# Kernel tuning notes

Measured on AMD Instinct MI355X. Metric: run time of the kernel, lower is better.

The kernel has to match this reference:

```python
import jax, jax.numpy as jnp
import numpy as np

N_NODES = 256
IN_FEATURES = 4096
OUT_FEATURES = 7
LAYERS = 4
WIRES = 8                      # ceil(log2(n_nodes))
DIM = 2 ** WIRES               # state-vector length = 256
P2 = WIRES * (WIRES - 1) // 2  # 28 controlled gates per block
N_W = 6 * WIRES + 3 * P2       # 132 weights per layer (matches weight_shape)
CPLX = jnp.complex64
# op2_all_layers ordering: gaps 1..w-1, then j
PAIRS = [(j, j + gap) for gap in range(1, WIRES) for j in range(WIRES - gap)]


def _ry(t):
    c, s = jnp.cos(t / 2), jnp.sin(t / 2)
    return jnp.stack([jnp.stack([c, -s]), jnp.stack([s, c])]).astype(CPLX)


def _rx(t):
    c = jnp.cos(t / 2).astype(CPLX)
    s = (-1j * jnp.sin(t / 2)).astype(CPLX)
    return jnp.stack([jnp.stack([c, s]), jnp.stack([s, c])])


def _rz(t):
    z = jnp.zeros((), CPLX)
    return jnp.stack([jnp.stack([jnp.exp(-0.5j * t).astype(CPLX), z]),
                      jnp.stack([z, jnp.exp(0.5j * t).astype(CPLX)])])


# Constant-angle gates (the source passes the integer weight index as the
# controlled-rotation angle, so these are compile-time numpy constants).
def _ry_np(a):
    c, s = np.cos(a / 2), np.sin(a / 2)
    return np.array([[c, -s], [s, c]], np.complex64)


def _rx_np(a):
    c, s = np.cos(a / 2), np.sin(a / 2)
    return np.array([[c, -1j * s], [-1j * s, c]], np.complex64)


def _rz_np(a):
    return np.diag([np.exp(-0.5j * a), np.exp(0.5j * a)]).astype(np.complex64)


def apply_1q(state, M, q):
    # state: [B] + [2]*WIRES; wire q lives on axis q+1 (wire 0 = MSB, PennyLane order)
    s = jnp.moveaxis(state, q + 1, -1)
    s = jnp.einsum('...b,ab->...a', s, M)
    return jnp.moveaxis(s, -1, q + 1)


def apply_c1q(state, M, c, t):
    # controlled gate: apply M on target wire t in the control==1 subspace
    s = jnp.moveaxis(state, (c + 1, t + 1), (-2, -1))
    s1 = jnp.einsum('...b,ab->...a', s[..., 1, :], M)
    s = jnp.stack([s[..., 0, :], s1], axis=-2)
    return jnp.moveaxis(s, (-2, -1), (c + 1, t + 1))


def q_layer(state, wv):
    # Faithful port of the source q_layer, including the quirk that the
    # CRY/CRX/CRZ angles are the integer running weight index (constants).
    wi = 0
    for q in range(WIRES):
        state = apply_1q(state, _ry(wv[wi + q]), q)
    wi += WIRES
    for i, (c, t) in enumerate(PAIRS):
        state = apply_c1q(state, _ry_np(float(wi + i)), c, t)
    wi += P2
    for q in range(WIRES):
        state = apply_1q(state, _ry(wv[wi + q]), q)
    wi += WIRES
    for q in range(WIRES):
        state = apply_1q(state, _rx(wv[wi + q]), q)
    wi += WIRES
    for i, (c, t) in enumerate(PAIRS):
        state = apply_c1q(state, _rx_np(float(wi + i)), c, t)
    wi += P2
    for q in range(WIRES):
        state = apply_1q(state, _rx(wv[wi + q]), q)
    wi += WIRES
    for q in range(WIRES):
        state = apply_1q(state, _rz(wv[wi + q]), q)
    wi += WIRES
    for i, (c, t) in enumerate(PAIRS):
        state = apply_c1q(state, _rz_np(float(wi + i)), c, t)
    wi += P2
    for q in range(WIRES):
        state = apply_1q(state, _rz(wv[wi + q]), q)
    return state


def circuit(samples, qweights):
    # samples: [B, N_NODES] real -> AmplitudeEmbedding(pad_with=0, normalize=True)
    B = samples.shape[0]
    v = samples
    if DIM > N_NODES:
        v = jnp.pad(v, ((0, 0), (0, DIM - N_NODES)))
    v = v / jnp.linalg.norm(v, axis=1, keepdims=True)
    state = v.astype(CPLX).reshape((B,) + (2,) * WIRES)
    layer = jax.checkpoint(q_layer)  # bounds residual memory under AD
    for l in range(LAYERS):
        state = layer(state, qweights[l])
    p = state.real ** 2 + state.imag ** 2  # probabilities, [B] + [2]*WIRES
    zs = []
    for q in range(WIRES):
        axes = tuple(a for a in range(1, WIRES + 1) if a != q + 1)
        m = p.sum(axis=axes)            # [B, 2]
        zs.append(m[:, 0] - m[:, 1])    # <Z_q> = P(0) - P(1)
    return jnp.stack(zs, axis=1)        # [B, WIRES]


def setup_inputs() -> dict:
    key = jax.random.key(0)
    k1, k2, k3, k4 = jax.random.split(key, 4)
    x = jax.random.normal(k1, (N_NODES, IN_FEATURES), jnp.float32)
    qweights = jax.random.uniform(k2, (LAYERS, N_W), jnp.float32, 0.0, 2.0 * np.pi)
    fc_w = jax.random.normal(k3, (OUT_FEATURES, WIRES), jnp.float32) / np.sqrt(WIRES)
    fc_b = jax.random.normal(k4, (OUT_FEATURES,), jnp.float32) / np.sqrt(WIRES)
    return {"x": x, "qweights": qweights, "fc_w": fc_w, "fc_b": fc_b}


def reference(x, qweights, fc_w, fc_b):
    z = circuit(x.T, qweights)      # [IN_FEATURES, WIRES]
    return z @ fc_w.T + fc_b        # [IN_FEATURES, OUT_FEATURES]
```

## Files before the change

kernel.cpp:

```cpp
#include <hip/hip_runtime.h>
#include <math.h>


namespace {

constexpr int NSAMP = 4096;
constexpr int NW_L  = 132;

constexpr double PI_D   = 3.14159265358979323846264338327950288;
constexpr double TWO_PI = 6.28318530717958647692528676655900577;

constexpr double red_pm_pi(double x) {
  double k = x / TWO_PI;
  long long ki = (long long)k;
  double r = x - (double)ki * TWO_PI;
  if (r > PI_D)  r -= TWO_PI;
  if (r < -PI_D) r += TWO_PI;
  return r;
}
constexpr double csin(double x) {
  double r = red_pm_pi(x), r2 = r * r, term = r, sum = r;
  for (int n = 1; n <= 13; ++n) { term *= -r2 / (double)((2*n)*(2*n+1)); sum += term; }
  return sum;
}
constexpr double ccos(double x) {
  double r = red_pm_pi(x), r2 = r * r, term = 1.0, sum = 1.0;
  for (int n = 1; n <= 13; ++n) { term *= -r2 / (double)((2*n-1)*(2*n)); sum += term; }
  return sum;
}

constexpr int PC[28] = {0,1,2,3,4,5,6, 0,1,2,3,4,5, 0,1,2,3,4, 0,1,2,3, 0,1,2, 0,1, 0};
constexpr int PT[28] = {1,2,3,4,5,6,7, 2,3,4,5,6,7, 3,4,5,6,7, 4,5,6,7, 5,6,7, 6,7, 7};

struct Tbl28 { float c[28]; float s[28]; };
constexpr Tbl28 mk_tbl(int base) {
  Tbl28 t{};
  for (int i = 0; i < 28; ++i) {
    double a = 0.5 * (double)(base + i);
    t.c[i] = (float)ccos(a);
    t.s[i] = (float)csin(a);
  }
  return t;
}
constexpr Tbl28 T_CRY = mk_tbl(8);
constexpr Tbl28 T_CRX = mk_tbl(52);

struct DTbl { float v[512]; };
constexpr DTbl mk_dcrz() {
  DTbl t{};
  for (int s = 0; s < 256; ++s) {
    double psi = 0.0;
    for (int i = 0; i < 28; ++i) {
      const int pc = 7 - PC[i], pt = 7 - PT[i];
      if ((s >> pc) & 1) {
        const double half = 0.5 * (double)(96 + i);
        psi += ((s >> pt) & 1) ? half : -half;
      }
    }
    t.v[2*s]   = (float)ccos(psi);
    t.v[2*s+1] = (float)csin(psi);
  }
  return t;
}
__device__ constexpr DTbl D_CRZ = mk_dcrz();

__device__ __forceinline__ float shx(float v, int sh) {
  if (sh == 0) {
    int r = __builtin_amdgcn_update_dpp((int)__float_as_uint(v), (int)__float_as_uint(v),
                                        0xB1, 0xF, 0xF, true);
    return __uint_as_float((unsigned)r);
  }
  if (sh == 1) {
    int r = __builtin_amdgcn_update_dpp((int)__float_as_uint(v), (int)__float_as_uint(v),
                                        0x4E, 0xF, 0xF, true);
    return __uint_as_float((unsigned)r);
  }
  return __shfl_xor(v, 1 << sh, 64);
}

__device__ __forceinline__ void gen_cross(float* ar, float* ai, int lane, int sh,
                                          float m00r, float m00i, float m01r, float m01i) {
  const int bbit = (lane >> sh) & 1;
  const float dr = m00r;
  const float di = bbit ? -m00i : m00i;
  const float g  = bbit ? -m01r : m01r;
  const float h  = m01i;
#pragma unroll
  for (int r = 0; r < 4; ++r) {
    float pr = shx(ar[r], sh);
    float pi = shx(ai[r], sh);
    float mr = ar[r], mi = ai[r];
    ar[r] = dr*mr - di*mi + g*pr - h*pi;
    ai[r] = dr*mi + di*mr + g*pi + h*pr;
  }
}
__device__ __forceinline__ void gen_local(float* ar, float* ai, int p,
                                          float m00r, float m00i, float m01r, float m01i) {
  const int m = 1 << p;
#pragma unroll
  for (int r0 = 0; r0 < 4; ++r0) {
    if (!(r0 & m)) {
      const int r1 = r0 | m;
      float a0r=ar[r0], a0i=ai[r0], a1r=ar[r1], a1i=ai[r1];
      ar[r0] =  m00r*a0r - m00i*a0i + m01r*a1r - m01i*a1i;
      ai[r0] =  m00r*a0i + m00i*a0r + m01r*a1i + m01i*a1r;
      ar[r1] = -m01r*a0r - m01i*a0i + m00r*a1r + m00i*a1i;
      ai[r1] = -m01r*a0i + m01i*a0r + m00r*a1i - m00i*a1r;
    }
  }
}
__device__ __forceinline__ void cry_cross(float* ar, float* ai, int lane,
                                          int shc, int sht, float cc, float sc) {
  const int ctrl = (lane >> shc) & 1;
  const float ce = ctrl ? cc : 1.0f;
  float se = ((lane >> sht) & 1) ? sc : -sc;
  se = ctrl ? se : 0.0f;
#pragma unroll
  for (int r = 0; r < 4; ++r) {
    float pr = shx(ar[r], sht);
    float pi = shx(ai[r], sht);
    ar[r] = ce*ar[r] + se*pr;
    ai[r] = ce*ai[r] + se*pi;
  }
}
__device__ __forceinline__ void cry_local(float* ar, float* ai, int lane,
                                          int shc, int pt, float cc, float sc) {
  const int ctrl = (lane >> shc) & 1;
  const float ce = ctrl ? cc : 1.0f;
  const float se = ctrl ? sc : 0.0f;
  const int m = 1 << pt;
#pragma unroll
  for (int r0 = 0; r0 < 4; ++r0) {
    if (!(r0 & m)) {
      const int r1 = r0 | m;
      float a0r=ar[r0], a0i=ai[r0], a1r=ar[r1], a1i=ai[r1];
      ar[r0] = ce*a0r - se*a1r;  ai[r0] = ce*a0i - se*a1i;
      ar[r1] = ce*a1r + se*a0r;  ai[r1] = ce*a1i + se*a0i;
    }
  }
}
__device__ __forceinline__ void ry_pair23(float* ar, float* ai, float cc, float sc) {
  float a0r=ar[2], a0i=ai[2], a1r=ar[3], a1i=ai[3];
  ar[2] = cc*a0r - sc*a1r;  ai[2] = cc*a0i - sc*a1i;
  ar[3] = cc*a1r + sc*a0r;  ai[3] = cc*a1i + sc*a0i;
}
__device__ __forceinline__ void crx_cross(float* ar, float* ai, int lane,
                                          int shc, int sht, float cc, float sc) {
  const int ctrl = (lane >> shc) & 1;
  const float ce = ctrl ? cc : 1.0f;
  const float se = ctrl ? sc : 0.0f;
#pragma unroll
  for (int r = 0; r < 4; ++r) {
    float pr = shx(ar[r], sht);
    float pi = shx(ai[r], sht);
    ar[r] = ce*ar[r] + se*pi;
    ai[r] = ce*ai[r] - se*pr;
  }
}
__device__ __forceinline__ void crx_local(float* ar, float* ai, int lane,
                                          int shc, int pt, float cc, float sc) {
  const int ctrl = (lane >> shc) & 1;
  const float ce = ctrl ? cc : 1.0f;
  const float se = ctrl ? sc : 0.0f;
  const int m = 1 << pt;
#pragma unroll
  for (int r0 = 0; r0 < 4; ++r0) {
    if (!(r0 & m)) {
      const int r1 = r0 | m;
      float a0r=ar[r0], a0i=ai[r0], a1r=ar[r1], a1i=ai[r1];
      ar[r0] = ce*a0r + se*a1i;  ai[r0] = ce*a0i - se*a1r;
      ar[r1] = ce*a1r + se*a0i;  ai[r1] = ce*a1i - se*a0r;
    }
  }
}
__device__ __forceinline__ void rx_pair23(float* ar, float* ai, float cc, float sc) {
  float a0r=ar[2], a0i=ai[2], a1r=ar[3], a1i=ai[3];
  ar[2] = cc*a0r + sc*a1i;  ai[2] = cc*a0i - sc*a1r;
  ar[3] = cc*a1r + sc*a0i;  ai[3] = cc*a1i - sc*a0r;
}

__device__ __forceinline__ unsigned short f2bf(float f) {
  unsigned int u = __float_as_uint(f);
  u = (u + 0x7FFFu + ((u >> 16) & 1u)) >> 16;
  return (unsigned short)u;
}

typedef __attribute__((ext_vector_type(8))) short bf16x8;
typedef __attribute__((ext_vector_type(4))) float f32x4;

}

__global__ __launch_bounds__(64) void build_half(const float* __restrict__ qw,
                                                 float* __restrict__ U1c,
                                                 float* __restrict__ U2c) {
  __shared__ float4 sM[48];
  const int lane = threadIdx.x;
  const int h    = blockIdx.x >> 8;
  const int s0   = blockIdx.x & 255;

  if (lane < 48) {
    const int lp  = lane / 24;
    const int rem = lane - lp * 24;
    const int j   = rem >> 3;
    const int q   = rem & 7;
    const int l   = 2 * h + lp;
    float a, bb;
    if (j == 0) {
      a  = qw[l * NW_L + q];
      bb = (l > 0) ? qw[(l - 1) * NW_L + 124 + q] : 0.f;
    } else if (j == 1) {
      a  = qw[l * NW_L + 44 + q];
      bb = qw[l * NW_L + 36 + q];
    } else {
      a  = (l < 3) ? qw[l * NW_L + 88 + q] : 0.f;
      bb = qw[l * NW_L + 80 + q];
    }
    float sa, ca, sb, cb;
    __sincosf(0.5f * a,  &sa, &ca);
    __sincosf(0.5f * bb, &sb, &cb);
    float4 m;
    if (j == 0)      m = make_float4(ca*cb, -ca*sb, -sa*cb, -sa*sb);
    else if (j == 1) m = make_float4(ca*cb, -sa*sb, -ca*sb, -sa*cb);
    else             m = make_float4(ca*cb, -sa*cb, -sb*sa, -sb*ca);
    sM[lane] = m;
  }

  float ar[4], ai[4];
#pragma unroll
  for (int r = 0; r < 4; ++r) {
    ar[r] = (((lane << 2) | r) == s0) ? 1.f : 0.f;
    ai[r] = 0.f;
  }
  float dzr[4], dzi[4];
#pragma unroll
  for (int r = 0; r < 4; ++r) {
    const int s = (lane << 2) | r;
    dzr[r] = D_CRZ.v[2*s];
    dzi[r] = D_CRZ.v[2*s+1];
  }
  __syncthreads();

#pragma unroll 1
  for (int lp = 0; lp < 2; ++lp) {
    const int base = lp * 24;
#pragma unroll
    for (int q = 0; q < 8; ++q) {
      float4 m = sM[base + q];
      if (q <= 5) gen_cross(ar, ai, lane, 5 - q, m.x, m.y, m.z, m.w);
      else        gen_local(ar, ai, 7 - q, m.x, m.y, m.z, m.w);
    }
#pragma unroll
    for (int i = 0; i < 28; ++i) {
      const int c = PC[i], t = PT[i];
      const float cc = T_CRY.c[i], sc = T_CRY.s[i];
      if (t <= 5)      cry_cross(ar, ai, lane, 5 - c, 5 - t, cc, sc);
      else if (c <= 5) cry_local(ar, ai, lane, 5 - c, 7 - t, cc, sc);
      else             ry_pair23(ar, ai, cc, sc);
    }
#pragma unroll
    for (int q = 0; q < 8; ++q) {
      float4 m = sM[base + 8 + q];
      if (q <= 5) gen_cross(ar, ai, lane, 5 - q, m.x, m.y, m.z, m.w);
      else        gen_local(ar, ai, 7 - q, m.x, m.y, m.z, m.w);
    }
#pragma unroll
    for (int i = 0; i < 28; ++i) {
      const int c = PC[i], t = PT[i];
      const float cc = T_CRX.c[i], sc = T_CRX.s[i];
      if (t <= 5)      crx_cross(ar, ai, lane, 5 - c, 5 - t, cc, sc);
      else if (c <= 5) crx_local(ar, ai, lane, 5 - c, 7 - t, cc, sc);
      else             rx_pair23(ar, ai, cc, sc);
    }
#pragma unroll
    for (int q = 0; q < 8; ++q) {
      float4 m = sM[base + 16 + q];
      if (q <= 5) gen_cross(ar, ai, lane, 5 - q, m.x, m.y, m.z, m.w);
      else        gen_local(ar, ai, 7 - q, m.x, m.y, m.z, m.w);
    }
    if (2 * h + lp < 3) {
#pragma unroll
      for (int r = 0; r < 4; ++r) {
        float mr = ar[r], mi = ai[r];
        ar[r] = mr*dzr[r] - mi*dzi[r];
        ai[r] = mr*dzi[r] + mi*dzr[r];
      }
    }
  }

  float* Uc = h ? U2c : U1c;
  float4* dst = (float4*)(Uc + (size_t)s0 * 512);
  dst[2*lane]     = make_float4(ar[0], ai[0], ar[1], ai[1]);
  dst[2*lane + 1] = make_float4(ar[2], ai[2], ar[3], ai[3]);
}

__global__ __launch_bounds__(256) void combine_u(const float* __restrict__ U1c,
                                                 const float* __restrict__ U2c,
                                                 unsigned short* __restrict__ Ubf) {
  __shared__ float2 S2[32 * 16];
  __shared__ float2 S1[16 * 33];
  const int tid = threadIdx.x;
  const int ti  = tid & 15;
  const int tj  = tid >> 4;
  const int bi  = blockIdx.x & 15;
  const int bj  = blockIdx.x >> 4;

  float accr = 0.f, acci = 0.f;
#pragma unroll 1
  for (int kt = 0; kt < 8; ++kt) {
    __syncthreads();
#pragma unroll
    for (int v = 0; v < 2; ++v) {
      const int s = v * 256 + tid;
      const int k  = s >> 4, i = s & 15;
      S2[k * 16 + i] = *(const float2*)(U2c + (size_t)(kt*32 + k) * 512 + (bi*16 + i) * 2);
      const int j2 = s >> 5, k2 = s & 31;
      S1[j2 * 33 + k2] = *(const float2*)(U1c + (size_t)(bj*16 + j2) * 512 + (kt*32 + k2) * 2);
    }
    __syncthreads();
#pragma unroll
    for (int kk = 0; kk < 32; ++kk) {
      const float2 a = S2[kk * 16 + ti];
      const float2 b = S1[tj * 33 + kk];
      accr = fmaf(a.x, b.x, accr);  accr = fmaf(-a.y, b.y, accr);
      acci = fmaf(a.x, b.y, acci);  acci = fmaf(a.y, b.x, acci);
    }
  }
  const int i = bi * 16 + ti, j = bj * 16 + tj;
  Ubf[(size_t)i * 256 + j]         = f2bf(accr);
  Ubf[(size_t)(i + 256) * 256 + j] = f2bf(acci);
}

__global__ __launch_bounds__(1024) void eval3(const float* __restrict__ x,
                                              const unsigned short* __restrict__ Ubf,
                                              const float* __restrict__ fcw,
                                              const float* __restrict__ fcb,
                                              float* __restrict__ out) {
  __shared__ unsigned short Xs[16 * 264];
  __shared__ float Zp[16][16][9];
  __shared__ float Zf[16][9];
  const int tid  = threadIdx.x;
  const int lane = tid & 63;
  const int w    = tid >> 6;
  const int colbase = blockIdx.x * 16;

  {
    const int k  = tid >> 2;
    const int c4 = (tid & 3) * 4;
    const float4 v = *(const float4*)(x + (size_t)k * NSAMP + colbase + c4);
    Xs[(c4 + 0) * 264 + k] = f2bf(v.x);
    Xs[(c4 + 1) * 264 + k] = f2bf(v.y);
    Xs[(c4 + 2) * 264 + k] = f2bf(v.z);
    Xs[(c4 + 3) * 264 + k] = f2bf(v.w);
  }
  __syncthreads();

  const int quad = lane >> 4;
  const int n    = lane & 15;
  const int rowb = w * 32;

  f32x4 acc[2];
  acc[0] = (f32x4){0.f, 0.f, 0.f, 0.f};
  acc[1] = (f32x4){0.f, 0.f, 0.f, 0.f};

#pragma unroll
  for (int kt = 0; kt < 8; ++kt) {
    const bf16x8 bfrag = *(const bf16x8*)&Xs[n * 264 + kt * 32 + quad * 8];
#pragma unroll
    for (int rt = 0; rt < 2; ++rt) {
      const int row = rowb + rt * 16 + n;
      const bf16x8 afrag = *(const bf16x8*)(Ubf + (size_t)row * 256 + kt * 32 + quad * 8);
      acc[rt] = __builtin_amdgcn_mfma_f32_16x16x32_bf16(afrag, bfrag, acc[rt], 0, 0, 0);
    }
  }

  float za[9];
#pragma unroll
  for (int i = 0; i < 9; ++i) za[i] = 0.f;
  const float m4 = (lane & 32) ? -1.f : 1.f;
  const float m5 = (lane & 16) ? -1.f : 1.f;
#pragma unroll
  for (int rt = 0; rt < 2; ++rt) {
#pragma unroll
    for (int reg = 0; reg < 4; ++reg) {
      const float v = acc[rt][reg];
      const float p = v * v;
      za[0] += p;
      za[1] += (w & 4)   ? -p : p;
      za[2] += (w & 2)   ? -p : p;
      za[3] += (w & 1)   ? -p : p;
      za[4] += rt        ? -p : p;
      za[5] = fmaf(m4, p, za[5]);
      za[6] = fmaf(m5, p, za[6]);
      za[7] += (reg & 2) ? -p : p;
      za[8] += (reg & 1) ? -p : p;
    }
  }
#pragma unroll
  for (int off = 16; off <= 32; off <<= 1) {
#pragma unroll
    for (int i = 0; i < 9; ++i) za[i] += __shfl_xor(za[i], off, 64);
  }
  if (lane < 16) {
#pragma unroll
    for (int i = 0; i < 9; ++i) Zp[w][lane][i] = za[i];
  }
  __syncthreads();

  if (tid < 144) {
    const int col = tid / 9, q = tid - col * 9;
    float z = 0.f;
#pragma unroll
    for (int ww = 0; ww < 16; ++ww) z += Zp[ww][col][q];
    Zf[col][q] = z;
  }
  __syncthreads();

  if (tid < 112) {
    const int col = tid / 7, oo = tid - col * 7;
    const float inv = 1.f / Zf[col][0];
    float v = fcb[oo];
#pragma unroll
    for (int q = 0; q < 8; ++q)
      v = fmaf(fcw[oo * 8 + q], Zf[col][1 + q] * inv, v);
    out[(size_t)(colbase + col) * 7 + oo] = v;
  }
}

extern "C" void kernel_launch(void* const* d_in, const int* in_sizes, int n_in,
                              void* d_out, int out_size, void* d_ws, size_t ws_size,
                              hipStream_t stream) {
  const float* x   = (const float*)d_in[0];
  const float* qw  = (const float*)d_in[1];
  const float* fcw = (const float*)d_in[2];
  const float* fcb = (const float*)d_in[3];
  float* out = (float*)d_out;

  float* U1c = (float*)d_ws;
  float* U2c = U1c + 256 * 512;
  unsigned short* Ubf = (unsigned short*)(U2c + 256 * 512);

  hipLaunchKernelGGL(build_half, dim3(512), dim3(64),   0, stream, qw, U1c, U2c);
  hipLaunchKernelGGL(combine_u,  dim3(256), dim3(256),  0, stream, U1c, U2c, Ubf);
  hipLaunchKernelGGL(eval3,      dim3(256), dim3(1024), 0, stream, x, Ubf, fcw, fcb, out);
}
```

Before: 94.84 us.

## Drop combine kernel by chaining two half-unitary GEMMs inside eval

Instead of multiplying the two half-circuit unitaries into a full unitary in a separate fp32 kernel, the build kernel now writes U1 as bf16 and U2 as a real 512x512 block matrix that encodes the complex product. The eval kernel applies U1 to the input tile with MFMA, stores the bf16 intermediate in shared memory, then applies the 512-wide W2. This removes one launch and the scalar fp32 complex matmul. In exchange, eval does three times the MFMA work and reads a larger matrix, and the extra bf16 rounding of the intermediate state adds error. The build kernel's transposed scattered 2-byte stores may also be poorly coalesced.

```diff
diff --git a/kernel.cpp b/kernel.cpp
--- a/kernel.cpp
+++ b/kernel.cpp
@@ -190,9 +190,9 @@
 
 }
 
-__global__ __launch_bounds__(64) void build_half(const float* __restrict__ qw,
-                                                 float* __restrict__ U1c,
-                                                 float* __restrict__ U2c) {
+__global__ __launch_bounds__(64) void build_emit(const float* __restrict__ qw,
+                                                 unsigned short* __restrict__ U1bf,
+                                                 unsigned short* __restrict__ W2bf) {
   __shared__ float4 sM[48];
   const int lane = threadIdx.x;
   const int h    = blockIdx.x >> 8;
@@ -287,55 +287,33 @@
     }
   }
 
-  float* Uc = h ? U2c : U1c;
-  float4* dst = (float4*)(Uc + (size_t)s0 * 512);
-  dst[2*lane]     = make_float4(ar[0], ai[0], ar[1], ai[1]);
-  dst[2*lane + 1] = make_float4(ar[2], ai[2], ar[3], ai[3]);
-}
-
-__global__ __launch_bounds__(256) void combine_u(const float* __restrict__ U1c,
-                                                 const float* __restrict__ U2c,
-                                                 unsigned short* __restrict__ Ubf) {
-  __shared__ float2 S2[32 * 16];
-  __shared__ float2 S1[16 * 33];
-  const int tid = threadIdx.x;
-  const int ti  = tid & 15;
-  const int tj  = tid >> 4;
-  const int bi  = blockIdx.x & 15;
-  const int bj  = blockIdx.x >> 4;
-
-  float accr = 0.f, acci = 0.f;
-#pragma unroll 1
-  for (int kt = 0; kt < 8; ++kt) {
-    __syncthreads();
-#pragma unroll
-    for (int v = 0; v < 2; ++v) {
-      const int s = v * 256 + tid;
-      const int k  = s >> 4, i = s & 15;
-      S2[k * 16 + i] = *(const float2*)(U2c + (size_t)(kt*32 + k) * 512 + (bi*16 + i) * 2);
-      const int j2 = s >> 5, k2 = s & 31;
-      S1[j2 * 33 + k2] = *(const float2*)(U1c + (size_t)(bj*16 + j2) * 512 + (kt*32 + k2) * 2);
-    }
-    __syncthreads();
-#pragma unroll
-    for (int kk = 0; kk < 32; ++kk) {
-      const float2 a = S2[kk * 16 + ti];
-      const float2 b = S1[tj * 33 + kk];
-      accr = fmaf(a.x, b.x, accr);  accr = fmaf(-a.y, b.y, accr);
-      acci = fmaf(a.x, b.y, acci);  acci = fmaf(a.y, b.x, acci);
-    }
-  }
-  const int i = bi * 16 + ti, j = bj * 16 + tj;
-  Ubf[(size_t)i * 256 + j]         = f2bf(accr);
-  Ubf[(size_t)(i + 256) * 256 + j] = f2bf(acci);
-}
-
-__global__ __launch_bounds__(1024) void eval3(const float* __restrict__ x,
-                                              const unsigned short* __restrict__ Ubf,
-                                              const float* __restrict__ fcw,
-                                              const float* __restrict__ fcb,
-                                              float* __restrict__ out) {
+  if (h == 0) {
+#pragma unroll
+    for (int r = 0; r < 4; ++r) {
+      const int o = (lane << 2) | r;
+      U1bf[(size_t)o * 256 + s0]         = f2bf(ar[r]);
+      U1bf[(size_t)(o + 256) * 256 + s0] = f2bf(ai[r]);
+    }
+  } else {
+#pragma unroll
+    for (int r = 0; r < 4; ++r) {
+      const int o = (lane << 2) | r;
+      W2bf[(size_t)o * 512 + s0]               = f2bf(ar[r]);
+      W2bf[(size_t)(o + 256) * 512 + s0]       = f2bf(ai[r]);
+      W2bf[(size_t)o * 512 + 256 + s0]         = f2bf(-ai[r]);
+      W2bf[(size_t)(o + 256) * 512 + 256 + s0] = f2bf(ar[r]);
+    }
+  }
+}
+
+__global__ __launch_bounds__(1024) void eval_chain(const float* __restrict__ x,
+                                                   const unsigned short* __restrict__ U1bf,
+                                                   const unsigned short* __restrict__ W2bf,
+                                                   const float* __restrict__ fcw,
+                                                   const float* __restrict__ fcb,
+                                                   float* __restrict__ out) {
   __shared__ unsigned short Xs[16 * 264];
+  __shared__ unsigned short Ys[16 * 520];
   __shared__ float Zp[16][16][9];
   __shared__ float Zf[16][9];
   const int tid  = threadIdx.x;
@@ -358,17 +336,40 @@
   const int n    = lane & 15;
   const int rowb = w * 32;
 
+  {
+    f32x4 a1[2];
+    a1[0] = (f32x4){0.f, 0.f, 0.f, 0.f};
+    a1[1] = (f32x4){0.f, 0.f, 0.f, 0.f};
+#pragma unroll
+    for (int kt = 0; kt < 8; ++kt) {
+      const bf16x8 bfrag = *(const bf16x8*)&Xs[n * 264 + kt * 32 + quad * 8];
+#pragma unroll
+      for (int rt = 0; rt < 2; ++rt) {
+        const int row = rowb + rt * 16 + n;
+        const bf16x8 afrag = *(const bf16x8*)(U1bf + (size_t)row * 256 + kt * 32 + quad * 8);
+        a1[rt] = __builtin_amdgcn_mfma_f32_16x16x32_bf16(afrag, bfrag, a1[rt], 0, 0, 0);
+      }
+    }
+#pragma unroll
+    for (int rt = 0; rt < 2; ++rt) {
+      unsigned short p4[4];
+#pragma unroll
+      for (int reg = 0; reg < 4; ++reg) p4[reg] = f2bf(a1[rt][reg]);
+      *(uint2*)&Ys[n * 520 + rowb + rt * 16 + quad * 4] = *(const uint2*)p4;
+    }
+  }
+  __syncthreads();
+
   f32x4 acc[2];
   acc[0] = (f32x4){0.f, 0.f, 0.f, 0.f};
   acc[1] = (f32x4){0.f, 0.f, 0.f, 0.f};
-
-#pragma unroll
-  for (int kt = 0; kt < 8; ++kt) {
-    const bf16x8 bfrag = *(const bf16x8*)&Xs[n * 264 + kt * 32 + quad * 8];
+#pragma unroll
+  for (int kt = 0; kt < 16; ++kt) {
+    const bf16x8 bfrag = *(const bf16x8*)&Ys[n * 520 + kt * 32 + quad * 8];
 #pragma unroll
     for (int rt = 0; rt < 2; ++rt) {
       const int row = rowb + rt * 16 + n;
-      const bf16x8 afrag = *(const bf16x8*)(Ubf + (size_t)row * 256 + kt * 32 + quad * 8);
+      const bf16x8 afrag = *(const bf16x8*)(W2bf + (size_t)row * 512 + kt * 32 + quad * 8);
       acc[rt] = __builtin_amdgcn_mfma_f32_16x16x32_bf16(afrag, bfrag, acc[rt], 0, 0, 0);
     }
   }
@@ -435,11 +436,10 @@
   const float* fcb = (const float*)d_in[3];
   float* out = (float*)d_out;
 
-  float* U1c = (float*)d_ws;
-  float* U2c = U1c + 256 * 512;
-  unsigned short* Ubf = (unsigned short*)(U2c + 256 * 512);
-
-  hipLaunchKernelGGL(build_half, dim3(512), dim3(64),   0, stream, qw, U1c, U2c);
-  hipLaunchKernelGGL(combine_u,  dim3(256), dim3(256),  0, stream, U1c, U2c, Ubf);
-  hipLaunchKernelGGL(eval3,      dim3(256), dim3(1024), 0, stream, x, Ubf, fcw, fcb, out);
-}
+  unsigned short* U1bf = (unsigned short*)d_ws;
+  unsigned short* W2bf = U1bf + (size_t)512 * 256;
+
+  hipLaunchKernelGGL(build_emit, dim3(512), dim3(64),   0, stream, qw, U1bf, W2bf);
+  hipLaunchKernelGGL(eval_chain, dim3(256), dim3(1024), 0, stream,
+                     x, U1bf, W2bf, fcw, fcb, out);
+}
```

New measurement: 100.8 us. 1.06x slower.

## Build unitary columns with one amplitude per thread across four wavefronts

Applied to the files above, without the earlier changes.

The unitary-building kernel moves from one 64-lane wavefront holding four amplitudes per lane to a 256-thread block holding one amplitude per thread. Exchanges on the low six wire bits use DPP, ds_swizzle or shuffle within a wave, and gates whose partner sits in another wave (bits 6 and 7) go through shared memory with two barriers each. This spreads the serial gate chain over more threads to cut per-thread latency, at the cost of many block-wide barriers and LDS round trips.

```diff
diff --git a/kernel.cpp b/kernel.cpp
--- a/kernel.cpp
+++ b/kernel.cpp
@@ -64,119 +64,100 @@
 }
 __device__ constexpr DTbl D_CRZ = mk_dcrz();
 
-__device__ __forceinline__ float shx(float v, int sh) {
-  if (sh == 0) {
+__device__ __forceinline__ float shx1(float v, int p) {
+  if (p == 0) {
     int r = __builtin_amdgcn_update_dpp((int)__float_as_uint(v), (int)__float_as_uint(v),
                                         0xB1, 0xF, 0xF, true);
     return __uint_as_float((unsigned)r);
   }
-  if (sh == 1) {
+  if (p == 1) {
     int r = __builtin_amdgcn_update_dpp((int)__float_as_uint(v), (int)__float_as_uint(v),
                                         0x4E, 0xF, 0xF, true);
     return __uint_as_float((unsigned)r);
   }
-  return __shfl_xor(v, 1 << sh, 64);
-}
-
-__device__ __forceinline__ void gen_cross(float* ar, float* ai, int lane, int sh,
-                                          float m00r, float m00i, float m01r, float m01i) {
-  const int bbit = (lane >> sh) & 1;
+  if (p == 2) return __uint_as_float((unsigned)__builtin_amdgcn_ds_swizzle(
+                      (int)__float_as_uint(v), 0x101F));
+  if (p == 3) return __uint_as_float((unsigned)__builtin_amdgcn_ds_swizzle(
+                      (int)__float_as_uint(v), 0x201F));
+  if (p == 4) return __uint_as_float((unsigned)__builtin_amdgcn_ds_swizzle(
+                      (int)__float_as_uint(v), 0x401F));
+  return __shfl_xor(v, 32, 64);
+}
+
+__device__ __forceinline__ void gen_lane(float& ar, float& ai, int s, int p,
+                                         float m00r, float m00i, float m01r, float m01i) {
+  const int b = (s >> p) & 1;
   const float dr = m00r;
-  const float di = bbit ? -m00i : m00i;
-  const float g  = bbit ? -m01r : m01r;
-  const float h  = m01i;
-#pragma unroll
-  for (int r = 0; r < 4; ++r) {
-    float pr = shx(ar[r], sh);
-    float pi = shx(ai[r], sh);
-    float mr = ar[r], mi = ai[r];
-    ar[r] = dr*mr - di*mi + g*pr - h*pi;
-    ai[r] = dr*mi + di*mr + g*pi + h*pr;
-  }
-}
-__device__ __forceinline__ void gen_local(float* ar, float* ai, int p,
-                                          float m00r, float m00i, float m01r, float m01i) {
-  const int m = 1 << p;
-#pragma unroll
-  for (int r0 = 0; r0 < 4; ++r0) {
-    if (!(r0 & m)) {
-      const int r1 = r0 | m;
-      float a0r=ar[r0], a0i=ai[r0], a1r=ar[r1], a1i=ai[r1];
-      ar[r0] =  m00r*a0r - m00i*a0i + m01r*a1r - m01i*a1i;
-      ai[r0] =  m00r*a0i + m00i*a0r + m01r*a1i + m01i*a1r;
-      ar[r1] = -m01r*a0r - m01i*a0i + m00r*a1r + m00i*a1i;
-      ai[r1] = -m01r*a0i + m01i*a0r + m00r*a1i - m00i*a1r;
-    }
-  }
-}
-__device__ __forceinline__ void cry_cross(float* ar, float* ai, int lane,
-                                          int shc, int sht, float cc, float sc) {
-  const int ctrl = (lane >> shc) & 1;
+  const float di = b ? -m00i : m00i;
+  const float g  = b ? -m01r : m01r;
+  const float hh = m01i;
+  const float pr = shx1(ar, p);
+  const float pi = shx1(ai, p);
+  const float mr = ar, mi = ai;
+  ar = dr*mr - di*mi + g*pr - hh*pi;
+  ai = dr*mi + di*mr + g*pi + hh*pr;
+}
+__device__ __forceinline__ void gen_xw(float& ar, float& ai, int s, int p,
+                                       float m00r, float m00i, float m01r, float m01i,
+                                       float2* xbuf) {
+  xbuf[s] = make_float2(ar, ai);
+  __syncthreads();
+  const float2 pt = xbuf[s ^ (1 << p)];
+  __syncthreads();
+  const int b = (s >> p) & 1;
+  const float dr = m00r;
+  const float di = b ? -m00i : m00i;
+  const float g  = b ? -m01r : m01r;
+  const float hh = m01i;
+  const float mr = ar, mi = ai;
+  ar = dr*mr - di*mi + g*pt.x - hh*pt.y;
+  ai = dr*mi + di*mr + g*pt.y + hh*pt.x;
+}
+__device__ __forceinline__ void cry_lane(float& ar, float& ai, int s, int pc, int pt,
+                                         float cc, float sc) {
+  const int ctrl = (s >> pc) & 1;
   const float ce = ctrl ? cc : 1.0f;
-  float se = ((lane >> sht) & 1) ? sc : -sc;
+  float se = ((s >> pt) & 1) ? sc : -sc;
   se = ctrl ? se : 0.0f;
-#pragma unroll
-  for (int r = 0; r < 4; ++r) {
-    float pr = shx(ar[r], sht);
-    float pi = shx(ai[r], sht);
-    ar[r] = ce*ar[r] + se*pr;
-    ai[r] = ce*ai[r] + se*pi;
-  }
-}
-__device__ __forceinline__ void cry_local(float* ar, float* ai, int lane,
-                                          int shc, int pt, float cc, float sc) {
-  const int ctrl = (lane >> shc) & 1;
+  const float pr = shx1(ar, pt);
+  const float pi = shx1(ai, pt);
+  ar = ce*ar + se*pr;
+  ai = ce*ai + se*pi;
+}
+__device__ __forceinline__ void cry_xw(float& ar, float& ai, int s, int pc, int pt,
+                                       float cc, float sc, float2* xbuf) {
+  xbuf[s] = make_float2(ar, ai);
+  __syncthreads();
+  const float2 p = xbuf[s ^ (1 << pt)];
+  __syncthreads();
+  const int ctrl = (s >> pc) & 1;
+  const float ce = ctrl ? cc : 1.0f;
+  float se = ((s >> pt) & 1) ? sc : -sc;
+  se = ctrl ? se : 0.0f;
+  ar = ce*ar + se*p.x;
+  ai = ce*ai + se*p.y;
+}
+__device__ __forceinline__ void crx_lane(float& ar, float& ai, int s, int pc, int pt,
+                                         float cc, float sc) {
+  const int ctrl = (s >> pc) & 1;
   const float ce = ctrl ? cc : 1.0f;
   const float se = ctrl ? sc : 0.0f;
-  const int m = 1 << pt;
-#pragma unroll
-  for (int r0 = 0; r0 < 4; ++r0) {
-    if (!(r0 & m)) {
-      const int r1 = r0 | m;
-      float a0r=ar[r0], a0i=ai[r0], a1r=ar[r1], a1i=ai[r1];
-      ar[r0] = ce*a0r - se*a1r;  ai[r0] = ce*a0i - se*a1i;
-      ar[r1] = ce*a1r + se*a0r;  ai[r1] = ce*a1i + se*a0i;
-    }
-  }
-}
-__device__ __forceinline__ void ry_pair23(float* ar, float* ai, float cc, float sc) {
-  float a0r=ar[2], a0i=ai[2], a1r=ar[3], a1i=ai[3];
-  ar[2] = cc*a0r - sc*a1r;  ai[2] = cc*a0i - sc*a1i;
-  ar[3] = cc*a1r + sc*a0r;  ai[3] = cc*a1i + sc*a0i;
-}
-__device__ __forceinline__ void crx_cross(float* ar, float* ai, int lane,
-                                          int shc, int sht, float cc, float sc) {
-  const int ctrl = (lane >> shc) & 1;
+  const float pr = shx1(ar, pt);
+  const float pi = shx1(ai, pt);
+  ar = ce*ar + se*pi;
+  ai = ce*ai - se*pr;
+}
+__device__ __forceinline__ void crx_xw(float& ar, float& ai, int s, int pc, int pt,
+                                       float cc, float sc, float2* xbuf) {
+  xbuf[s] = make_float2(ar, ai);
+  __syncthreads();
+  const float2 p = xbuf[s ^ (1 << pt)];
+  __syncthreads();
+  const int ctrl = (s >> pc) & 1;
   const float ce = ctrl ? cc : 1.0f;
   const float se = ctrl ? sc : 0.0f;
-#pragma unroll
-  for (int r = 0; r < 4; ++r) {
-    float pr = shx(ar[r], sht);
-    float pi = shx(ai[r], sht);
-    ar[r] = ce*ar[r] + se*pi;
-    ai[r] = ce*ai[r] - se*pr;
-  }
-}
-__device__ __forceinline__ void crx_local(float* ar, float* ai, int lane,
-                                          int shc, int pt, float cc, float sc) {
-  const int ctrl = (lane >> shc) & 1;
-  const float ce = ctrl ? cc : 1.0f;
-  const float se = ctrl ? sc : 0.0f;
-  const int m = 1 << pt;
-#pragma unroll
-  for (int r0 = 0; r0 < 4; ++r0) {
-    if (!(r0 & m)) {
-      const int r1 = r0 | m;
-      float a0r=ar[r0], a0i=ai[r0], a1r=ar[r1], a1i=ai[r1];
-      ar[r0] = ce*a0r + se*a1i;  ai[r0] = ce*a0i - se*a1r;
-      ar[r1] = ce*a1r + se*a0i;  ai[r1] = ce*a1i - se*a0r;
-    }
-  }
-}
-__device__ __forceinline__ void rx_pair23(float* ar, float* ai, float cc, float sc) {
-  float a0r=ar[2], a0i=ai[2], a1r=ar[3], a1i=ai[3];
-  ar[2] = cc*a0r + sc*a1i;  ai[2] = cc*a0i - sc*a1r;
-  ar[3] = cc*a1r + sc*a0i;  ai[3] = cc*a1i - sc*a0r;
+  ar = ce*ar + se*p.y;
+  ai = ce*ai - se*p.x;
 }
 
 __device__ __forceinline__ unsigned short f2bf(float f) {
@@ -190,17 +171,19 @@
 
 }
 
-__global__ __launch_bounds__(64) void build_half(const float* __restrict__ qw,
-                                                 float* __restrict__ U1c,
-                                                 float* __restrict__ U2c) {
+__global__ __launch_bounds__(256) void build_half4w(const float* __restrict__ qw,
+                                                    float* __restrict__ U1c,
+                                                    float* __restrict__ U2c) {
   __shared__ float4 sM[48];
-  const int lane = threadIdx.x;
-  const int h    = blockIdx.x >> 8;
-  const int s0   = blockIdx.x & 255;
-
-  if (lane < 48) {
-    const int lp  = lane / 24;
-    const int rem = lane - lp * 24;
+  __shared__ float2 xbuf[256];
+  const int tid = threadIdx.x;
+  const int h   = blockIdx.x >> 8;
+  const int s0  = blockIdx.x & 255;
+  const int s   = tid;
+
+  if (tid < 48) {
+    const int lp  = tid / 24;
+    const int rem = tid - lp * 24;
     const int j   = rem >> 3;
     const int q   = rem & 7;
     const int l   = 2 * h + lp;
@@ -222,22 +205,13 @@
     if (j == 0)      m = make_float4(ca*cb, -ca*sb, -sa*cb, -sa*sb);
     else if (j == 1) m = make_float4(ca*cb, -sa*sb, -ca*sb, -sa*cb);
     else             m = make_float4(ca*cb, -sa*cb, -sb*sa, -sb*ca);
-    sM[lane] = m;
-  }
-
-  float ar[4], ai[4];
-#pragma unroll
-  for (int r = 0; r < 4; ++r) {
-    ar[r] = (((lane << 2) | r) == s0) ? 1.f : 0.f;
-    ai[r] = 0.f;
-  }
-  float dzr[4], dzi[4];
-#pragma unroll
-  for (int r = 0; r < 4; ++r) {
-    const int s = (lane << 2) | r;
-    dzr[r] = D_CRZ.v[2*s];
-    dzi[r] = D_CRZ.v[2*s+1];
-  }
+    sM[tid] = m;
+  }
+
+  float ar = (s == s0) ? 1.f : 0.f;
+  float ai = 0.f;
+  const float dzr = D_CRZ.v[2*s];
+  const float dzi = D_CRZ.v[2*s+1];
   __syncthreads();
 
 #pragma unroll 1
@@ -246,51 +220,47 @@
 #pragma unroll
     for (int q = 0; q < 8; ++q) {
       float4 m = sM[base + q];
-      if (q <= 5) gen_cross(ar, ai, lane, 5 - q, m.x, m.y, m.z, m.w);
-      else        gen_local(ar, ai, 7 - q, m.x, m.y, m.z, m.w);
+      if (q == 0)      gen_xw(ar, ai, s, 7, m.x, m.y, m.z, m.w, xbuf);
+      else if (q == 1) gen_xw(ar, ai, s, 6, m.x, m.y, m.z, m.w, xbuf);
+      else             gen_lane(ar, ai, s, 7 - q, m.x, m.y, m.z, m.w);
     }
 #pragma unroll
     for (int i = 0; i < 28; ++i) {
-      const int c = PC[i], t = PT[i];
+      const int pc = 7 - PC[i], pt = 7 - PT[i];
       const float cc = T_CRY.c[i], sc = T_CRY.s[i];
-      if (t <= 5)      cry_cross(ar, ai, lane, 5 - c, 5 - t, cc, sc);
-      else if (c <= 5) cry_local(ar, ai, lane, 5 - c, 7 - t, cc, sc);
-      else             ry_pair23(ar, ai, cc, sc);
+      if (pt == 6) cry_xw(ar, ai, s, pc, pt, cc, sc, xbuf);
+      else         cry_lane(ar, ai, s, pc, pt, cc, sc);
     }
 #pragma unroll
     for (int q = 0; q < 8; ++q) {
       float4 m = sM[base + 8 + q];
-      if (q <= 5) gen_cross(ar, ai, lane, 5 - q, m.x, m.y, m.z, m.w);
-      else        gen_local(ar, ai, 7 - q, m.x, m.y, m.z, m.w);
+      if (q == 0)      gen_xw(ar, ai, s, 7, m.x, m.y, m.z, m.w, xbuf);
+      else if (q == 1) gen_xw(ar, ai, s, 6, m.x, m.y, m.z, m.w, xbuf);
+      else             gen_lane(ar, ai, s, 7 - q, m.x, m.y, m.z, m.w);
     }
 #pragma unroll
     for (int i = 0; i < 28; ++i) {
-      const int c = PC[i], t = PT[i];
+      const int pc = 7 - PC[i], pt = 7 - PT[i];
       const float cc = T_CRX.c[i], sc = T_CRX.s[i];
-      if (t <= 5)      crx_cross(ar, ai, lane, 5 - c, 5 - t, cc, sc);
-      else if (c <= 5) crx_local(ar, ai, lane, 5 - c, 7 - t, cc, sc);
-      else             rx_pair23(ar, ai, cc, sc);
+      if (pt == 6) crx_xw(ar, ai, s, pc, pt, cc, sc, xbuf);
+      else         crx_lane(ar, ai, s, pc, pt, cc, sc);
     }
 #pragma unroll
     for (int q = 0; q < 8; ++q) {
       float4 m = sM[base + 16 + q];
-      if (q <= 5) gen_cross(ar, ai, lane, 5 - q, m.x, m.y, m.z, m.w);
-      else        gen_local(ar, ai, 7 - q, m.x, m.y, m.z, m.w);
+      if (q == 0)      gen_xw(ar, ai, s, 7, m.x, m.y, m.z, m.w, xbuf);
+      else if (q == 1) gen_xw(ar, ai, s, 6, m.x, m.y, m.z, m.w, xbuf);
+      else             gen_lane(ar, ai, s, 7 - q, m.x, m.y, m.z, m.w);
     }
     if (2 * h + lp < 3) {
-#pragma unroll
-      for (int r = 0; r < 4; ++r) {
-        float mr = ar[r], mi = ai[r];
-        ar[r] = mr*dzr[r] - mi*dzi[r];
-        ai[r] = mr*dzi[r] + mi*dzr[r];
-      }
+      const float mr = ar, mi = ai;
+      ar = mr*dzr - mi*dzi;
+      ai = mr*dzi + mi*dzr;
     }
   }
 
   float* Uc = h ? U2c : U1c;
-  float4* dst = (float4*)(Uc + (size_t)s0 * 512);
-  dst[2*lane]     = make_float4(ar[0], ai[0], ar[1], ai[1]);
-  dst[2*lane + 1] = make_float4(ar[2], ai[2], ar[3], ai[3]);
+  ((float2*)(Uc + (size_t)s0 * 512))[s] = make_float2(ar, ai);
 }
 
 __global__ __launch_bounds__(256) void combine_u(const float* __restrict__ U1c,
@@ -439,7 +409,7 @@
   float* U2c = U1c + 256 * 512;
   unsigned short* Ubf = (unsigned short*)(U2c + 256 * 512);
 
-  hipLaunchKernelGGL(build_half, dim3(512), dim3(64),   0, stream, qw, U1c, U2c);
-  hipLaunchKernelGGL(combine_u,  dim3(256), dim3(256),  0, stream, U1c, U2c, Ubf);
-  hipLaunchKernelGGL(eval3,      dim3(256), dim3(1024), 0, stream, x, Ubf, fcw, fcb, out);
-}
+  hipLaunchKernelGGL(build_half4w, dim3(512), dim3(256),  0, stream, qw, U1c, U2c);
+  hipLaunchKernelGGL(combine_u,    dim3(256), dim3(256),  0, stream, U1c, U2c, Ubf);
+  hipLaunchKernelGGL(eval3,        dim3(256), dim3(1024), 0, stream, x, Ubf, fcw, fcb, out);
+}
```

New measurement: 89.28 us. -5.9%, faster.
